# Performance work log

Measured on AMD Instinct MI355X. Metric: run time of the kernel, lower is better.

Reference implementation:

```python
import jax, jax.numpy as jnp
import numpy as np

N_VISITS, N_PROC, N_MED = 64, 32, 16
V_DIAG, V_PROC, V_MED = 2000, 1500, 4000
EMB, EMB_FF = 256, 128


def _normalize(adj):
    # row-normalize(adj + I), matching GCN.normalize
    adj = adj + np.eye(adj.shape[0], dtype=np.float32)
    rs = adj.sum(1)
    rinv = np.where(rs > 0, 1.0 / rs, 0.0).astype(np.float32)
    return (adj * rinv[:, None]).astype(np.float32)


def setup_inputs() -> dict:
    key = jax.random.key(0)
    ks = jax.random.split(key, 24)
    rng = np.random.default_rng(0)
    ehr = (rng.random((V_MED, V_MED)) < 0.01).astype(np.float32)
    ddi = (rng.random((V_MED, V_MED)) < 0.01).astype(np.float32)
    s = 0.02
    return {
        'proc_codes': jax.random.randint(ks[0], (N_VISITS, N_PROC), 0, V_DIAG + V_PROC + 2),
        'med_codes': jax.random.randint(ks[1], (N_VISITS, N_MED), 0, V_MED),
        'emb_table': jax.random.normal(ks[2], (V_DIAG + V_PROC + 2, EMB_FF)) * s,
        'conv_w': jax.random.normal(ks[3], (3,)) * 0.3,
        'conv_b': jnp.zeros((1,)),
        'wq': jax.random.normal(ks[4], (EMB_FF, EMB)) * s,
        'wk': jax.random.normal(ks[5], (EMB_FF, EMB)) * s,
        'wv': jax.random.normal(ks[6], (EMB_FF, EMB)) * s,
        'wr': jax.random.normal(ks[7], (EMB, EMB)) * s,
        'alpha': jax.random.normal(ks[8], (EMB,)),
        'beta': jax.random.normal(ks[9], (EMB,)),
        'ehr_adj_norm': jnp.asarray(_normalize(ehr)),
        'ddi_adj_norm': jnp.asarray(_normalize(ddi)),
        'ddi_adj_raw': jnp.asarray(ddi),
        'ehr_w1': jax.random.normal(ks[10], (V_MED, EMB)) * s,
        'ehr_b1': jnp.zeros((EMB,)),
        'ehr_w2': jax.random.normal(ks[11], (EMB, EMB)) * s,
        'ehr_b2': jnp.zeros((EMB,)),
        'ddi_w1': jax.random.normal(ks[12], (V_MED, EMB)) * s,
        'ddi_b1': jnp.zeros((EMB,)),
        'ddi_w2': jax.random.normal(ks[13], (EMB, EMB)) * s,
        'ddi_b2': jnp.zeros((EMB,)),
        'inter': jax.random.normal(ks[14], (1,)) * 0.1,
        'out_w1': jax.random.normal(ks[15], (3 * EMB, 2 * EMB)) * s,
        'out_b1': jnp.zeros((2 * EMB,)),
        'out_w2': jax.random.normal(ks[16], (2 * EMB, V_MED)) * s,
        'out_b2': jnp.zeros((V_MED,)),
    }


def _fastformer(x, wq, wk, wv, wr, alpha, beta):
    # x: (1, n, EMB_FF); additive linear attention (all-ones mask => no-op)
    q = x @ wq  # (1, n, EMB)
    k = x @ wk
    v = x @ wv
    scale = EMB ** -0.5
    aw = jax.nn.softmax(q * alpha * scale, axis=-1)
    gq = jnp.sum(q * aw, axis=1)              # global query (1, EMB)
    p = gq[:, None, :] * k                    # (1, n, EMB)
    bw = jax.nn.softmax(p * beta * scale, axis=-1)
    gk = jnp.sum(p * bw, axis=1)              # global key (1, EMB)
    return (gk[:, None, :] * v) @ wr + q


def _gcn(adj, w1, b1, w2, b2):
    # input x = I, so first layer support is just w1
    h = jax.nn.relu(adj @ w1 + b1)
    return adj @ (h @ w2) + b2


def reference(proc_codes, med_codes, emb_table, conv_w, conv_b, wq, wk, wv, wr, alpha, beta,
              ehr_adj_norm, ddi_adj_norm, ddi_adj_raw,
              ehr_w1, ehr_b1, ehr_w2, ehr_b2, ddi_w1, ddi_b1, ddi_w2, ddi_b2,
              inter, out_w1, out_b1, out_w2, out_b2):
    n = proc_codes.shape[0]
    # per-admission mean embedding  (n, EMB_FF)
    i2 = emb_table[proc_codes].mean(axis=1)
    # Conv1d(1,1,k=3,same) over the feature dim, then ReLU
    xp = jnp.pad(i2, ((0, 0), (1, 1)))
    i2 = jax.nn.relu(conv_w[0] * xp[:, :-2] + conv_w[1] * xp[:, 1:-1] + conv_w[2] * xp[:, 2:] + conv_b)
    feat = _fastformer(i2[None], wq, wk, wv, wr, alpha, beta)[0]  # (n, EMB)
    query = feat[-1:]
    drug_memory = _gcn(ehr_adj_norm, ehr_w1, ehr_b1, ehr_w2, ehr_b2) \
        - _gcn(ddi_adj_norm, ddi_w1, ddi_b1, ddi_w2, ddi_b2) * inter[0]
    key_w1 = jax.nn.softmax(query @ drug_memory.T, axis=-1)   # (1, V_MED)
    fact1 = key_w1 @ drug_memory                              # (1, EMB)
    # history (len(input) > 1): multi-hot med history values
    history_keys = feat[:-1]
    hv = jnp.zeros((n - 1, V_MED), dtype=feat.dtype)
    hv = hv.at[jnp.arange(n - 1)[:, None], med_codes[:-1]].set(1.0)
    visit_w = jax.nn.softmax(query @ history_keys.T, axis=-1)
    fact2 = (visit_w @ hv) @ drug_memory
    h = jnp.concatenate([query, fact1, fact2], axis=-1)       # (1, 3*EMB)
    result = jax.nn.relu(h @ out_w1 + out_b1) @ out_w2 + out_b2
    sp = jax.nn.sigmoid(result)[0]
    batch_neg = 0.0005 * jnp.einsum('i,ij,j->', sp, ddi_adj_raw, sp)
    return result, batch_neg
```

## Files before the change

kernel.cpp:

```cpp
#include <hip/hip_runtime.h>
#include <hip/hip_bf16.h>

#define NV 64
#define NP 32
#define NM 16
#define VMED 4000
#define EMB 256
#define EMBFF 128
#define CAP 128


__device__ __forceinline__ float block_sum_256(float v, float* red) {
    int t = threadIdx.x;
    red[t] = v; __syncthreads();
    for (int s = 128; s > 0; s >>= 1) { if (t < s) red[t] += red[t + s]; __syncthreads(); }
    float r = red[0]; __syncthreads();
    return r;
}
__device__ __forceinline__ float block_max_256(float v, float* red) {
    int t = threadIdx.x;
    red[t] = v; __syncthreads();
    for (int s = 128; s > 0; s >>= 1) { if (t < s) red[t] = fmaxf(red[t], red[t + s]); __syncthreads(); }
    float r = red[0]; __syncthreads();
    return r;
}

__global__ void k_ff1(const int* __restrict__ proc, const float* __restrict__ emb,
                      const float* __restrict__ cw, const float* __restrict__ cb,
                      const float* __restrict__ wq, const float* __restrict__ wk,
                      const float* __restrict__ wv, const float* __restrict__ alpha,
                      float* __restrict__ q, float* __restrict__ k, float* __restrict__ v,
                      float* __restrict__ qaw) {
    __shared__ float sm[EMBFF + 2];
    __shared__ float x[EMBFF];
    __shared__ float red[256];
    int vi = blockIdx.x, t = threadIdx.x;
    if (t < EMBFF) {
        float s = 0.f;
        for (int c = 0; c < NP; c++) s += emb[proc[vi * NP + c] * EMBFF + t];
        sm[t + 1] = s * (1.0f / NP);
    }
    if (t == 0) { sm[0] = 0.f; sm[EMBFF + 1] = 0.f; }
    __syncthreads();
    if (t < EMBFF) {
        float o = cw[0] * sm[t] + cw[1] * sm[t + 1] + cw[2] * sm[t + 2] + cb[0];
        x[t] = o > 0.f ? o : 0.f;
    }
    __syncthreads();
    float aq = 0, ak = 0, av = 0;
    for (int e = 0; e < EMBFF; e++) {
        float xe = x[e];
        aq += xe * wq[e * EMB + t];
        ak += xe * wk[e * EMB + t];
        av += xe * wv[e * EMB + t];
    }
    q[vi * EMB + t] = aq; k[vi * EMB + t] = ak; v[vi * EMB + t] = av;
    const float scale = 0.0625f;
    float z = aq * alpha[t] * scale;
    float m = block_max_256(z, red);
    float e_ = __expf(z - m);
    float sum = block_sum_256(e_, red);
    qaw[vi * EMB + t] = aq * (e_ / sum);
}

__global__ void k_pbw(const float* __restrict__ qaw, const float* __restrict__ k,
                      const float* __restrict__ beta, float* __restrict__ pbw) {
    __shared__ float red[256];
    int vi = blockIdx.x, f = threadIdx.x;
    float g = 0;
    for (int r = 0; r < NV; r++) g += qaw[r * EMB + f];
    float p = g * k[vi * EMB + f];
    const float scale = 0.0625f;
    float z = p * beta[f] * scale;
    float m = block_max_256(z, red);
    float e_ = __expf(z - m);
    float sum = block_sum_256(e_, red);
    pbw[vi * EMB + f] = p * (e_ / sum);
}

__global__ void k_feat(const float* __restrict__ pbw, const float* __restrict__ v,
                       const float* __restrict__ q, const float* __restrict__ wr,
                       float* __restrict__ feat) {
    __shared__ float s[EMB];
    int vi = blockIdx.x, f = threadIdx.x;
    float g = 0;
    for (int r = 0; r < NV; r++) g += pbw[r * EMB + f];
    s[f] = g * v[vi * EMB + f];
    __syncthreads();
    float acc = 0;
    for (int e = 0; e < EMB; e++) acc += s[e] * wr[e * EMB + f];
    feat[vi * EMB + f] = acc + q[vi * EMB + f];
}

__global__ void k_visitw_wmed(const float* __restrict__ feat, const int* __restrict__ med,
                              float* __restrict__ w_med) {
    __shared__ float qs[EMB];
    __shared__ float vw[64];
    __shared__ float red[256];
    __shared__ float wm[VMED];
    int t = threadIdx.x;
    for (int e = t; e < EMB; e += 256) qs[e] = feat[63 * EMB + e];
    for (int i = t; i < VMED; i += 256) wm[i] = 0.f;
    __syncthreads();
    float sc = -1e30f;
    if (t < 63) {
        float a = 0;
        for (int e = 0; e < EMB; e++) a += qs[e] * feat[t * EMB + e];
        sc = a;
    }
    float m = block_max_256(sc, red);
    float e_ = (t < 63) ? __expf(sc - m) : 0.f;
    float sum = block_sum_256(e_, red);
    if (t < 63) vw[t] = e_ / sum;
    __syncthreads();
    for (int i = t; i < 63 * NM; i += 256) {
        int vv = i / NM, mm = i % NM;
        int code = med[vv * NM + mm];
        bool dup = false;
        for (int m2 = 0; m2 < mm; m2++)
            if (med[vv * NM + m2] == code) dup = true;
        if (!dup) atomicAdd(&wm[code], vw[vv]);
    }
    __syncthreads();
    for (int i = t; i < VMED; i += 256) w_med[i] = wm[i];
}

__global__ void k_qproj(const float* __restrict__ ew2, const float* __restrict__ dw2,
                        const float* __restrict__ b2e, const float* __restrict__ b2d,
                        const float* __restrict__ feat,
                        float* __restrict__ qE, float* __restrict__ qD,
                        float* __restrict__ cc) {
    __shared__ float red[256];
    int b = blockIdx.x, t = threadIdx.x;
    const float* q = feat + 63 * EMB;
    float val;
    if (b < 256)      val = ew2[b * EMB + t] * q[t];
    else if (b < 512) val = dw2[(b - 256) * EMB + t] * q[t];
    else if (b == 512) val = b2e[t] * q[t];
    else               val = b2d[t] * q[t];
    float s = block_sum_256(val, red);
    if (t == 0) {
        if (b < 256) qE[b] = s;
        else if (b < 512) qD[b - 256] = s;
        else if (b == 512) cc[0] = s;
        else cc[1] = s;
    }
}

__global__ void k_scan(const float* __restrict__ eadj, const float* __restrict__ draw,
                       int* __restrict__ ccntE, int* __restrict__ cidxE, float* __restrict__ cvalE,
                       int* __restrict__ ccntD, int* __restrict__ cidxD, float* __restrict__ cvalD) {
    __shared__ int idx[CAP];
    __shared__ float val[CAP];
    __shared__ int cnt;
    int b = blockIdx.x, t = threadIdx.x;
    bool isD = b >= VMED;
    int i = isD ? b - VMED : b;
    const float* adj = isD ? draw : eadj;
    int*   ccnt = isD ? ccntD : ccntE;
    int*   cidx = isD ? cidxD : cidxE;
    float* cval = isD ? cvalD : cvalE;
    if (t == 0) cnt = 0;
    const float4* row4 = (const float4*)(adj + (size_t)i * VMED);
    float4 a0 = row4[t];
    float4 a1 = row4[t + 256];
    float4 a2 = row4[t + 512];
    float4 a3 = (t < VMED / 4 - 768) ? row4[t + 768] : make_float4(0.f, 0.f, 0.f, 0.f);
    asm volatile("" :: "v"(a0.x), "v"(a0.y), "v"(a0.z), "v"(a0.w),
                       "v"(a1.x), "v"(a1.y), "v"(a1.z), "v"(a1.w),
                       "v"(a2.x), "v"(a2.y), "v"(a2.z), "v"(a2.w),
                       "v"(a3.x), "v"(a3.y), "v"(a3.z), "v"(a3.w));
    __syncthreads();
    #define PROC(A, C0) \
        if (A.x != 0.f) { int p = atomicAdd(&cnt, 1); if (p < CAP) { idx[p] = (C0);     val[p] = A.x; } } \
        if (A.y != 0.f) { int p = atomicAdd(&cnt, 1); if (p < CAP) { idx[p] = (C0) + 1; val[p] = A.y; } } \
        if (A.z != 0.f) { int p = atomicAdd(&cnt, 1); if (p < CAP) { idx[p] = (C0) + 2; val[p] = A.z; } } \
        if (A.w != 0.f) { int p = atomicAdd(&cnt, 1); if (p < CAP) { idx[p] = (C0) + 3; val[p] = A.w; } }
    PROC(a0, t * 4)
    PROC(a1, (t + 256) * 4)
    PROC(a2, (t + 512) * 4)
    PROC(a3, (t + 768) * 4)
    #undef PROC
    __syncthreads();
    int n;
    float rinv = 0.f;
    if (isD) {
        int n_raw = cnt < CAP - 1 ? cnt : CAP - 1;
        n = n_raw + 1;
        rinv = 1.0f / (float)n;
        if (t == n_raw) { idx[t] = i; }
    } else {
        n = cnt < CAP ? cnt : CAP;
    }
    __syncthreads();
    int n8 = (n + 7) & ~7;
    if (t == 0) ccnt[i] = n;
    if (t < n)       { cidx[i * CAP + t] = idx[t]; cval[i * CAP + t] = isD ? rinv : val[t]; }
    else if (t < n8) { cidx[i * CAP + t] = 0;      cval[i * CAP + t] = 0.f; }
}

__global__ void k_gat(const int* __restrict__ ccntE, const int* __restrict__ cidxE,
                      const float* __restrict__ cvalE,
                      const int* __restrict__ ccntD, const int* __restrict__ cidxD,
                      const float* __restrict__ cvalD,
                      const float* __restrict__ ew1, const float* __restrict__ eb1,
                      const float* __restrict__ dw1, const float* __restrict__ db1,
                      float* __restrict__ hE, float* __restrict__ hD) {
    int b = blockIdx.x, t = threadIdx.x;
    bool isD = (b & 4) != 0;
    int rank = (b >> 3) * 4 + (b & 3);
    const int*   ccnt = isD ? ccntD : ccntE;
    const int*   cidx = isD ? cidxD : cidxE;
    const float* cval = isD ? cvalD : cvalE;
    const float* w1   = isD ? dw1 : ew1;
    const float* b1   = isD ? db1 : eb1;
    float* h = isD ? hD : hE;
    int r0 = rank * 4;
    for (int r = 0; r < 4; r++) {
        int base = (r0 + r) * CAP;
        int n8 = (ccnt[r0 + r] + 7) & ~7;
        float acc = b1[t];
        for (int e = 0; e < n8; e += 8) {
            int i0 = cidx[base + e];     float v0 = cval[base + e];
            int i1 = cidx[base + e + 1]; float v1 = cval[base + e + 1];
            int i2 = cidx[base + e + 2]; float v2 = cval[base + e + 2];
            int i3 = cidx[base + e + 3]; float v3 = cval[base + e + 3];
            int i4 = cidx[base + e + 4]; float v4 = cval[base + e + 4];
            int i5 = cidx[base + e + 5]; float v5 = cval[base + e + 5];
            int i6 = cidx[base + e + 6]; float v6 = cval[base + e + 6];
            int i7 = cidx[base + e + 7]; float v7 = cval[base + e + 7];
            acc += v0 * w1[(size_t)i0 * EMB + t] + v1 * w1[(size_t)i1 * EMB + t]
                 + v2 * w1[(size_t)i2 * EMB + t] + v3 * w1[(size_t)i3 * EMB + t]
                 + v4 * w1[(size_t)i4 * EMB + t] + v5 * w1[(size_t)i5 * EMB + t]
                 + v6 * w1[(size_t)i6 * EMB + t] + v7 * w1[(size_t)i7 * EMB + t];
        }
        h[(size_t)(r0 + r) * EMB + t] = acc > 0.f ? acc : 0.f;
    }
}

__global__ void k_u(const float* __restrict__ hE, const float* __restrict__ hD,
                    const float* __restrict__ qE, const float* __restrict__ qD,
                    const float* __restrict__ wm,
                    float* __restrict__ uE, float* __restrict__ uD,
                    float* __restrict__ vbuf, float* __restrict__ swm) {
    __shared__ float red[256];
    int b = blockIdx.x, t = threadIdx.x;
    if (b < 2000) {
        int w = t >> 6, lane = t & 63;
        int j = b * 4 + w;
        const float* row; const float* qv; float* uo;
        if (j < VMED) { row = hE + (size_t)j * EMB; qv = qE; uo = uE + j; }
        else { row = hD + (size_t)(j - VMED) * EMB; qv = qD; uo = uD + (j - VMED); }
        float4 hv = *(const float4*)(row + lane * 4);
        float4 qq = *(const float4*)(qv + lane * 4);
        float s = hv.x * qq.x + hv.y * qq.y + hv.z * qq.z + hv.w * qq.w;
        for (int off = 32; off > 0; off >>= 1) s += __shfl_down(s, off, 64);
        if (lane == 0) *uo = s;
    } else if (b < 2063) {
        int idx = (b - 2000) * 256 + t;
        if (idx < 16000) vbuf[idx] = 0.f;
    } else {
        float s = 0;
        for (int i = t; i < VMED; i += 256) s += wm[i];
        s = block_sum_256(s, red);
        if (t == 0) swm[0] = s;
    }
}

__global__ void k_sdm(const int* __restrict__ ccntE, const int* __restrict__ cidxE,
                      const float* __restrict__ cvalE,
                      const int* __restrict__ ccntD, const int* __restrict__ cidxD,
                      const float* __restrict__ cvalD,
                      const float* __restrict__ uE, const float* __restrict__ uD,
                      const float* __restrict__ cc, const float* __restrict__ inter,
                      float* __restrict__ sdm) {
    int t = threadIdx.x;
    int i = blockIdx.x * 4 + (t >> 6), lane = t & 63;
    int nE = ccntE[i];
    float sE = 0.f;
    for (int e = lane; e < nE; e += 64) sE += cvalE[i * CAP + e] * uE[cidxE[i * CAP + e]];
    int nD = ccntD[i];
    float sD = 0.f;
    for (int e = lane; e < nD; e += 64) sD += cvalD[i * CAP + e] * uD[cidxD[i * CAP + e]];
    for (int off = 32; off > 0; off >>= 1) {
        sE += __shfl_down(sE, off, 64);
        sD += __shfl_down(sD, off, 64);
    }
    if (lane == 0) sdm[i] = (sE + cc[0]) - inter[0] * (sD + cc[1]);
}

__global__ void k_softmax4000(const float* __restrict__ s, float* __restrict__ out) {
    __shared__ float red[256];
    int t = threadIdx.x;
    float m = -1e30f;
    for (int i = t; i < VMED; i += 256) m = fmaxf(m, s[i]);
    m = block_max_256(m, red);
    float sum = 0;
    for (int i = t; i < VMED; i += 256) { float e = __expf(s[i] - m); out[i] = e; sum += e; }
    sum = block_sum_256(sum, red);
    float inv = 1.f / sum;
    for (int i = t; i < VMED; i += 256) out[i] *= inv;
}

__global__ void k_scatter(const int* __restrict__ ccntE, const int* __restrict__ cidxE,
                          const float* __restrict__ cvalE,
                          const int* __restrict__ ccntD, const int* __restrict__ cidxD,
                          const float* __restrict__ cvalD,
                          const float* __restrict__ kw, const float* __restrict__ wm,
                          float* __restrict__ vE, float* __restrict__ v2E,
                          float* __restrict__ vD, float* __restrict__ v2D) {
    int t = threadIdx.x;
    int i = blockIdx.x * 4 + (t >> 6), lane = t & 63;
    float kwi = kw[i], wmi = wm[i];
    int nE = ccntE[i];
    for (int e = lane; e < nE; e += 64) {
        int j = cidxE[i * CAP + e];
        float v = cvalE[i * CAP + e];
        atomicAdd(&vE[j], kwi * v);
        atomicAdd(&v2E[j], wmi * v);
    }
    int nD = ccntD[i];
    for (int e = lane; e < nD; e += 64) {
        int j = cidxD[i * CAP + e];
        float v = cvalD[i * CAP + e];
        atomicAdd(&vD[j], kwi * v);
        atomicAdd(&v2D[j], wmi * v);
    }
}

__global__ void k_wsum(const float* __restrict__ hE, const float* __restrict__ hD,
                       const float* __restrict__ vE, const float* __restrict__ v2E,
                       const float* __restrict__ vD, const float* __restrict__ v2D,
                       float* __restrict__ pe1, float* __restrict__ pe2,
                       float* __restrict__ pd1, float* __restrict__ pd2) {
    int f = threadIdx.x, b = blockIdx.x;
    float a1 = 0, a2 = 0, a3 = 0, a4 = 0;
    int j0 = b * 100;
    for (int j = j0; j < j0 + 100; j++) {
        float he = hE[(size_t)j * EMB + f];
        float hd = hD[(size_t)j * EMB + f];
        a1 += vE[j] * he; a2 += v2E[j] * he;
        a3 += vD[j] * hd; a4 += v2D[j] * hd;
    }
    pe1[b * EMB + f] = a1; pe2[b * EMB + f] = a2;
    pd1[b * EMB + f] = a3; pd2[b * EMB + f] = a4;
}

__global__ void k_facts_final(const float* __restrict__ pe1, const float* __restrict__ pe2,
                              const float* __restrict__ pd1, const float* __restrict__ pd2,
                              const float* __restrict__ ew2, const float* __restrict__ dw2,
                              const float* __restrict__ b2e, const float* __restrict__ b2d,
                              const float* __restrict__ inter, const float* __restrict__ swm,
                              float* __restrict__ fact1, float* __restrict__ fact2) {
    __shared__ float gA[EMB];
    __shared__ float gB[EMB];
    int b = blockIdx.x, t = threadIdx.x;
    const float* pa = (b == 0) ? pe1 : pe2;
    const float* pb = (b == 0) ? pd1 : pd2;
    float s1 = 0, s2 = 0;
    for (int p = 0; p < 40; p++) { s1 += pa[p * EMB + t]; s2 += pb[p * EMB + t]; }
    gA[t] = s1; gB[t] = s2;
    __syncthreads();
    float accE = 0, accD = 0;
    for (int e = 0; e < EMB; e++) {
        accE += gA[e] * ew2[e * EMB + t];
        accD += gB[e] * dw2[e * EMB + t];
    }
    float bs = (b == 0) ? 1.f : swm[0];
    float r = accE + bs * b2e[t] - inter[0] * (accD + bs * b2d[t]);
    if (b == 0) fact1[t] = r; else fact2[t] = r;
}

__global__ void k_hidden_part(const float* __restrict__ feat, const float* __restrict__ fact1,
                              const float* __restrict__ fact2, const float* __restrict__ w1,
                              float* __restrict__ hpart) {
    __shared__ float xs[16];
    int b = blockIdx.x, t = threadIdx.x;
    int e0 = b * 16;
    if (t < 16) {
        int e = e0 + t;
        float xv;
        if (e < 256) xv = feat[63 * EMB + e];
        else if (e < 512) xv = fact1[e - 256];
        else              xv = fact2[e - 512];
        xs[t] = xv;
    }
    __syncthreads();
    float a1 = 0, a2 = 0;
    #pragma unroll
    for (int i = 0; i < 16; i++) {
        int e = e0 + i;
        a1 += xs[i] * w1[e * 512 + t];
        a2 += xs[i] * w1[e * 512 + t + 256];
    }
    hpart[b * 512 + t] = a1;
    hpart[b * 512 + t + 256] = a2;
}

__global__ void k_result(const float* __restrict__ hpart, const float* __restrict__ b1,
                         const float* __restrict__ w2, const float* __restrict__ b2,
                         float* __restrict__ out, float* __restrict__ sp) {
    __shared__ float hx[512];
    __shared__ float red[8][32];
    int t = threadIdx.x;
    for (int jj = t; jj < 512; jj += 256) {
        float s = b1[jj];
        for (int p = 0; p < 48; p++) s += hpart[p * 512 + jj];
        hx[jj] = s > 0.f ? s : 0.f;
    }
    __syncthreads();
    int lane = t & 31, seg = t >> 5;
    int j = blockIdx.x * 32 + lane;
    float acc = 0;
    int e0 = seg * 64;
    #pragma unroll 8
    for (int e = e0; e < e0 + 64; e++) acc += hx[e] * w2[(size_t)e * VMED + j];
    red[seg][lane] = acc;
    __syncthreads();
    if (seg == 0) {
        float s = b2[j];
        for (int p = 0; p < 8; p++) s += red[p][lane];
        out[j] = s;
        sp[j] = 1.f / (1.f + __expf(-s));
    }
}

__global__ void k_bneg(const int* __restrict__ ccntD, const int* __restrict__ cidxD,
                       const float* __restrict__ sp, float* __restrict__ bpart) {
    int wv = threadIdx.x >> 6, lane = threadIdx.x & 63;
    int i = blockIdx.x * 4 + wv;
    int n = ccntD[i] - 1;
    float s = 0.f;
    for (int e = lane; e < n; e += 64) s += sp[cidxD[i * CAP + e]];
    for (int off = 32; off > 0; off >>= 1) s += __shfl_down(s, off, 64);
    if (lane == 0) bpart[i] = sp[i] * s;
}

__global__ void FastRx_wo_Diag_19473381720179_kernel(const float* __restrict__ bpart,
                                                     float* __restrict__ out) {
    __shared__ float red[256];
    int t = threadIdx.x;
    float s = 0;
    for (int i = t; i < VMED; i += 256) s += bpart[i];
    s = block_sum_256(s, red);
    if (t == 0) out[VMED] = 0.0005f * s;
}

extern "C" __attribute__((visibility("default")))
void kernel_launch(void* const* d_in, const int* in_sizes, int n_in,
                   void* d_out, int out_size, void* d_ws, size_t ws_size,
                   hipStream_t stream) {
    const int*   proc_codes = (const int*)d_in[0];
    const int*   med_codes  = (const int*)d_in[1];
    const float* emb_table  = (const float*)d_in[2];
    const float* conv_w     = (const float*)d_in[3];
    const float* conv_b     = (const float*)d_in[4];
    const float* wq         = (const float*)d_in[5];
    const float* wk         = (const float*)d_in[6];
    const float* wv         = (const float*)d_in[7];
    const float* wr         = (const float*)d_in[8];
    const float* alpha      = (const float*)d_in[9];
    const float* beta       = (const float*)d_in[10];
    const float* ehr_adj    = (const float*)d_in[11];
    const float* ddi_adj    = (const float*)d_in[12];
    const float* ddi_raw    = (const float*)d_in[13];
    const float* ehr_w1     = (const float*)d_in[14];
    const float* ehr_b1     = (const float*)d_in[15];
    const float* ehr_w2     = (const float*)d_in[16];
    const float* ehr_b2     = (const float*)d_in[17];
    const float* ddi_w1     = (const float*)d_in[18];
    const float* ddi_b1     = (const float*)d_in[19];
    const float* ddi_w2     = (const float*)d_in[20];
    const float* ddi_b2     = (const float*)d_in[21];
    const float* inter      = (const float*)d_in[22];
    const float* out_w1     = (const float*)d_in[23];
    const float* out_b1     = (const float*)d_in[24];
    const float* out_w2     = (const float*)d_in[25];
    const float* out_b2     = (const float*)d_in[26];
    float* out = (float*)d_out;

    float* w = (float*)d_ws;
    float* q      = w;
    float* k      = w + 16384;
    float* v      = w + 32768;
    float* tmpA   = w + 49152;
    float* tmpB   = w + 65536;
    float* feat   = w + 81920;
    float* wmed   = w + 98304;
    float* sdm    = w + 102400;
    float* sp     = w + 106496;
    float* bufA   = w + 110592;
    float* bufC   = bufA + 1024000;
    float* bufB   = bufC + 1024000;
    int*   ccntE  = (int*)(bufB + 1024000);
    int*   cidxE  = ccntE + 4096;
    float* cvalE  = (float*)(cidxE + 512000);
    int*   ccntD  = (int*)(cvalE + 512000);
    int*   cidxD  = ccntD + 4096;
    float* cvalD  = (float*)(cidxD + 512000);
    float* qE   = bufB;
    float* qD   = bufB + 256;
    float* cc   = bufB + 512;
    float* swm  = bufB + 514;
    float* uE   = bufB + 1024;
    float* uD   = bufB + 5120;
    float* vbuf = bufB + 10240;
    float* vE   = vbuf;
    float* v2E  = vbuf + 4000;
    float* vD   = vbuf + 8000;
    float* v2D  = vbuf + 12000;
    float* pe1  = bufB + 26624;
    float* pe2  = bufB + 36864;
    float* pd1  = bufB + 47104;
    float* pd2  = bufB + 57344;
    float* fact1  = bufA;
    float* fact2  = bufA + 256;
    float* hpart  = bufA + 20480;
    float* bpart  = bufA + 45056;

    k_ff1<<<NV, EMB, 0, stream>>>(proc_codes, emb_table, conv_w, conv_b,
                                  wq, wk, wv, alpha, q, k, v, tmpA);
    k_pbw<<<NV, EMB, 0, stream>>>(tmpA, k, beta, tmpB);
    k_feat<<<NV, EMB, 0, stream>>>(tmpB, v, q, wr, feat);
    k_visitw_wmed<<<1, 256, 0, stream>>>(feat, med_codes, wmed);
    k_qproj<<<514, 256, 0, stream>>>(ehr_w2, ddi_w2, ehr_b2, ddi_b2, feat, qE, qD, cc);

    k_scan<<<2 * VMED, 256, 0, stream>>>(ehr_adj, ddi_raw,
                                         ccntE, cidxE, cvalE, ccntD, cidxD, cvalD);
    k_gat<<<2000, 256, 0, stream>>>(ccntE, cidxE, cvalE, ccntD, cidxD, cvalD,
                                    ehr_w1, ehr_b1, ddi_w1, ddi_b1,
                                    bufA, bufC);
    k_u<<<2064, 256, 0, stream>>>(bufA, bufC, qE, qD, wmed, uE, uD, vbuf, swm);
    k_sdm<<<1000, 256, 0, stream>>>(ccntE, cidxE, cvalE, ccntD, cidxD, cvalD,
                                    uE, uD, cc, inter, sdm);
    k_softmax4000<<<1, 256, 0, stream>>>(sdm, sdm);
    k_scatter<<<1000, 256, 0, stream>>>(ccntE, cidxE, cvalE, ccntD, cidxD, cvalD,
                                        sdm, wmed, vE, v2E, vD, v2D);
    k_wsum<<<40, 256, 0, stream>>>(bufA, bufC, vE, v2E, vD, v2D, pe1, pe2, pd1, pd2);
    k_facts_final<<<2, 256, 0, stream>>>(pe1, pe2, pd1, pd2, ehr_w2, ddi_w2,
                                         ehr_b2, ddi_b2, inter, swm, fact1, fact2);
    k_hidden_part<<<48, 256, 0, stream>>>(feat, fact1, fact2, out_w1, hpart);
    k_result<<<125, 256, 0, stream>>>(hpart, out_b1, out_w2, out_b2, out, sp);
    k_bneg<<<VMED / 4, 256, 0, stream>>>(ccntD, cidxD, sp, bpart);
    FastRx_wo_Diag_19473381720179_kernel<<<1, 256, 0, stream>>>(bpart, out);
}
```

Before: 402.4 us.

## Fuse small kernels to cut launch count and split wsum across more blocks

Merges visit-weight/med-weight and query projection into one k_mid launch, which also zeroes vbuf and computes the wm sum. The u dot products move into k_gat's epilogue through a block reduction, so k_u goes away. k_hidden_part is folded into k_result, where all 125 blocks recompute the 768x512 hidden layer redundantly. k_wsum is split into 160 blocks, one accumulator each. The aim is to remove launch overhead and raise parallelism, at the cost of redundant hidden-layer work and extra syncs in k_gat.

```diff
diff --git a/kernel.cpp b/kernel.cpp
--- a/kernel.cpp
+++ b/kernel.cpp
@@ -92,58 +92,65 @@
     feat[vi * EMB + f] = acc + q[vi * EMB + f];
 }
 
-__global__ void k_visitw_wmed(const float* __restrict__ feat, const int* __restrict__ med,
-                              float* __restrict__ w_med) {
+__global__ void k_mid(const float* __restrict__ feat, const int* __restrict__ med,
+                      const float* __restrict__ ew2, const float* __restrict__ dw2,
+                      const float* __restrict__ b2e, const float* __restrict__ b2d,
+                      float* __restrict__ w_med, float* __restrict__ swm,
+                      float* __restrict__ qE, float* __restrict__ qD,
+                      float* __restrict__ cc, float* __restrict__ vbuf) {
     __shared__ float qs[EMB];
     __shared__ float vw[64];
     __shared__ float red[256];
     __shared__ float wm[VMED];
-    int t = threadIdx.x;
-    for (int e = t; e < EMB; e += 256) qs[e] = feat[63 * EMB + e];
-    for (int i = t; i < VMED; i += 256) wm[i] = 0.f;
-    __syncthreads();
-    float sc = -1e30f;
-    if (t < 63) {
-        float a = 0;
-        for (int e = 0; e < EMB; e++) a += qs[e] * feat[t * EMB + e];
-        sc = a;
-    }
-    float m = block_max_256(sc, red);
-    float e_ = (t < 63) ? __expf(sc - m) : 0.f;
-    float sum = block_sum_256(e_, red);
-    if (t < 63) vw[t] = e_ / sum;
-    __syncthreads();
-    for (int i = t; i < 63 * NM; i += 256) {
-        int vv = i / NM, mm = i % NM;
-        int code = med[vv * NM + mm];
-        bool dup = false;
-        for (int m2 = 0; m2 < mm; m2++)
-            if (med[vv * NM + m2] == code) dup = true;
-        if (!dup) atomicAdd(&wm[code], vw[vv]);
-    }
-    __syncthreads();
-    for (int i = t; i < VMED; i += 256) w_med[i] = wm[i];
-}
-
-__global__ void k_qproj(const float* __restrict__ ew2, const float* __restrict__ dw2,
-                        const float* __restrict__ b2e, const float* __restrict__ b2d,
-                        const float* __restrict__ feat,
-                        float* __restrict__ qE, float* __restrict__ qD,
-                        float* __restrict__ cc) {
-    __shared__ float red[256];
     int b = blockIdx.x, t = threadIdx.x;
-    const float* q = feat + 63 * EMB;
-    float val;
-    if (b < 256)      val = ew2[b * EMB + t] * q[t];
-    else if (b < 512) val = dw2[(b - 256) * EMB + t] * q[t];
-    else if (b == 512) val = b2e[t] * q[t];
-    else               val = b2d[t] * q[t];
-    float s = block_sum_256(val, red);
-    if (t == 0) {
-        if (b < 256) qE[b] = s;
-        else if (b < 512) qD[b - 256] = s;
-        else if (b == 512) cc[0] = s;
-        else cc[1] = s;
+    if (b == 0) {
+        for (int e = t; e < EMB; e += 256) qs[e] = feat[63 * EMB + e];
+        for (int i = t; i < VMED; i += 256) wm[i] = 0.f;
+        __syncthreads();
+        float sc = -1e30f;
+        if (t < 63) {
+            float a = 0;
+            for (int e = 0; e < EMB; e++) a += qs[e] * feat[t * EMB + e];
+            sc = a;
+        }
+        float m = block_max_256(sc, red);
+        float e_ = (t < 63) ? __expf(sc - m) : 0.f;
+        float sum = block_sum_256(e_, red);
+        if (t < 63) vw[t] = e_ / sum;
+        __syncthreads();
+        for (int i = t; i < 63 * NM; i += 256) {
+            int vv = i / NM, mm = i % NM;
+            int code = med[vv * NM + mm];
+            bool dup = false;
+            for (int m2 = 0; m2 < mm; m2++)
+                if (med[vv * NM + m2] == code) dup = true;
+            if (!dup) atomicAdd(&wm[code], vw[vv]);
+        }
+        __syncthreads();
+        for (int i = t; i < VMED; i += 256) w_med[i] = wm[i];
+        __syncthreads();
+        float s = 0;
+        for (int i = t; i < VMED; i += 256) s += wm[i];
+        s = block_sum_256(s, red);
+        if (t == 0) swm[0] = s;
+    } else if (b <= 514) {
+        int bb = b - 1;
+        const float* q = feat + 63 * EMB;
+        float val;
+        if (bb < 256)       val = ew2[bb * EMB + t] * q[t];
+        else if (bb < 512)  val = dw2[(bb - 256) * EMB + t] * q[t];
+        else if (bb == 512) val = b2e[t] * q[t];
+        else                val = b2d[t] * q[t];
+        float s = block_sum_256(val, red);
+        if (t == 0) {
+            if (bb < 256) qE[bb] = s;
+            else if (bb < 512) qD[bb - 256] = s;
+            else if (bb == 512) cc[0] = s;
+            else cc[1] = s;
+        }
+    } else {
+        int idx = (b - 515) * 256 + t;
+        if (idx < 16000) vbuf[idx] = 0.f;
     }
 }
 
@@ -205,7 +212,10 @@
                       const float* __restrict__ cvalD,
                       const float* __restrict__ ew1, const float* __restrict__ eb1,
                       const float* __restrict__ dw1, const float* __restrict__ db1,
-                      float* __restrict__ hE, float* __restrict__ hD) {
+                      const float* __restrict__ qE, const float* __restrict__ qD,
+                      float* __restrict__ hE, float* __restrict__ hD,
+                      float* __restrict__ uE, float* __restrict__ uD) {
+    __shared__ float red[256];
     int b = blockIdx.x, t = threadIdx.x;
     bool isD = (b & 4) != 0;
     int rank = (b >> 3) * 4 + (b & 3);
@@ -215,6 +225,8 @@
     const float* w1   = isD ? dw1 : ew1;
     const float* b1   = isD ? db1 : eb1;
     float* h = isD ? hD : hE;
+    float* u = isD ? uD : uE;
+    float qt = (isD ? qD : qE)[t];
     int r0 = rank * 4;
     for (int r = 0; r < 4; r++) {
         int base = (r0 + r) * CAP;
@@ -234,36 +246,10 @@
                  + v4 * w1[(size_t)i4 * EMB + t] + v5 * w1[(size_t)i5 * EMB + t]
                  + v6 * w1[(size_t)i6 * EMB + t] + v7 * w1[(size_t)i7 * EMB + t];
         }
-        h[(size_t)(r0 + r) * EMB + t] = acc > 0.f ? acc : 0.f;
-    }
-}
-
-__global__ void k_u(const float* __restrict__ hE, const float* __restrict__ hD,
-                    const float* __restrict__ qE, const float* __restrict__ qD,
-                    const float* __restrict__ wm,
-                    float* __restrict__ uE, float* __restrict__ uD,
-                    float* __restrict__ vbuf, float* __restrict__ swm) {
-    __shared__ float red[256];
-    int b = blockIdx.x, t = threadIdx.x;
-    if (b < 2000) {
-        int w = t >> 6, lane = t & 63;
-        int j = b * 4 + w;
-        const float* row; const float* qv; float* uo;
-        if (j < VMED) { row = hE + (size_t)j * EMB; qv = qE; uo = uE + j; }
-        else { row = hD + (size_t)(j - VMED) * EMB; qv = qD; uo = uD + (j - VMED); }
-        float4 hv = *(const float4*)(row + lane * 4);
-        float4 qq = *(const float4*)(qv + lane * 4);
-        float s = hv.x * qq.x + hv.y * qq.y + hv.z * qq.z + hv.w * qq.w;
-        for (int off = 32; off > 0; off >>= 1) s += __shfl_down(s, off, 64);
-        if (lane == 0) *uo = s;
-    } else if (b < 2063) {
-        int idx = (b - 2000) * 256 + t;
-        if (idx < 16000) vbuf[idx] = 0.f;
-    } else {
-        float s = 0;
-        for (int i = t; i < VMED; i += 256) s += wm[i];
-        s = block_sum_256(s, red);
-        if (t == 0) swm[0] = s;
+        float hr = acc > 0.f ? acc : 0.f;
+        h[(size_t)(r0 + r) * EMB + t] = hr;
+        float s = block_sum_256(hr * qt, red);
+        if (t == 0) u[r0 + r] = s;
     }
 }
 
@@ -334,16 +320,18 @@
                        float* __restrict__ pe1, float* __restrict__ pe2,
                        float* __restrict__ pd1, float* __restrict__ pd2) {
     int f = threadIdx.x, b = blockIdx.x;
-    float a1 = 0, a2 = 0, a3 = 0, a4 = 0;
-    int j0 = b * 100;
-    for (int j = j0; j < j0 + 100; j++) {
-        float he = hE[(size_t)j * EMB + f];
-        float hd = hD[(size_t)j * EMB + f];
-        a1 += vE[j] * he; a2 += v2E[j] * he;
-        a3 += vD[j] * hd; a4 += v2D[j] * hd;
-    }
-    pe1[b * EMB + f] = a1; pe2[b * EMB + f] = a2;
-    pd1[b * EMB + f] = a3; pd2[b * EMB + f] = a4;
+    int a = b / 40, chunk = b % 40;
+    const float* h; const float* v; float* p;
+    if (a == 0)      { h = hE; v = vE;  p = pe1; }
+    else if (a == 1) { h = hE; v = v2E; p = pe2; }
+    else if (a == 2) { h = hD; v = vD;  p = pd1; }
+    else             { h = hD; v = v2D; p = pd2; }
+    float acc = 0;
+    int j0 = chunk * 100;
+    #pragma unroll 4
+    for (int j = j0; j < j0 + 100; j++)
+        acc += v[j] * h[(size_t)j * EMB + f];
+    p[chunk * EMB + f] = acc;
 }
 
 __global__ void k_facts_final(const float* __restrict__ pe1, const float* __restrict__ pe2,
@@ -371,41 +359,29 @@
     if (b == 0) fact1[t] = r; else fact2[t] = r;
 }
 
-__global__ void k_hidden_part(const float* __restrict__ feat, const float* __restrict__ fact1,
-                              const float* __restrict__ fact2, const float* __restrict__ w1,
-                              float* __restrict__ hpart) {
-    __shared__ float xs[16];
-    int b = blockIdx.x, t = threadIdx.x;
-    int e0 = b * 16;
-    if (t < 16) {
-        int e = e0 + t;
-        float xv;
-        if (e < 256) xv = feat[63 * EMB + e];
-        else if (e < 512) xv = fact1[e - 256];
-        else              xv = fact2[e - 512];
-        xs[t] = xv;
-    }
-    __syncthreads();
-    float a1 = 0, a2 = 0;
-    #pragma unroll
-    for (int i = 0; i < 16; i++) {
-        int e = e0 + i;
-        a1 += xs[i] * w1[e * 512 + t];
-        a2 += xs[i] * w1[e * 512 + t + 256];
-    }
-    hpart[b * 512 + t] = a1;
-    hpart[b * 512 + t + 256] = a2;
-}
-
-__global__ void k_result(const float* __restrict__ hpart, const float* __restrict__ b1,
+__global__ void k_result(const float* __restrict__ feat, const float* __restrict__ fact1,
+                         const float* __restrict__ fact2, const float* __restrict__ w1,
+                         const float* __restrict__ b1,
                          const float* __restrict__ w2, const float* __restrict__ b2,
                          float* __restrict__ out, float* __restrict__ sp) {
+    __shared__ float xs[768];
     __shared__ float hx[512];
     __shared__ float red[8][32];
     int t = threadIdx.x;
+    xs[t] = feat[63 * EMB + t];
+    xs[256 + t] = fact1[t];
+    xs[512 + t] = fact2[t];
+    __syncthreads();
     for (int jj = t; jj < 512; jj += 256) {
         float s = b1[jj];
-        for (int p = 0; p < 48; p++) s += hpart[p * 512 + jj];
+        for (int p = 0; p < 48; p++) {
+            int e0 = p * 16;
+            float partial = 0;
+            #pragma unroll
+            for (int i = 0; i < 16; i++)
+                partial += xs[e0 + i] * w1[(e0 + i) * 512 + jj];
+            s += partial;
+        }
         hx[jj] = s > 0.f ? s : 0.f;
     }
     __syncthreads();
@@ -515,32 +491,30 @@
     float* pd2  = bufB + 57344;
     float* fact1  = bufA;
     float* fact2  = bufA + 256;
-    float* hpart  = bufA + 20480;
     float* bpart  = bufA + 45056;
 
     k_ff1<<<NV, EMB, 0, stream>>>(proc_codes, emb_table, conv_w, conv_b,
                                   wq, wk, wv, alpha, q, k, v, tmpA);
     k_pbw<<<NV, EMB, 0, stream>>>(tmpA, k, beta, tmpB);
     k_feat<<<NV, EMB, 0, stream>>>(tmpB, v, q, wr, feat);
-    k_visitw_wmed<<<1, 256, 0, stream>>>(feat, med_codes, wmed);
-    k_qproj<<<514, 256, 0, stream>>>(ehr_w2, ddi_w2, ehr_b2, ddi_b2, feat, qE, qD, cc);
+    k_mid<<<578, 256, 0, stream>>>(feat, med_codes, ehr_w2, ddi_w2, ehr_b2, ddi_b2,
+                                   wmed, swm, qE, qD, cc, vbuf);
 
     k_scan<<<2 * VMED, 256, 0, stream>>>(ehr_adj, ddi_raw,
                                          ccntE, cidxE, cvalE, ccntD, cidxD, cvalD);
     k_gat<<<2000, 256, 0, stream>>>(ccntE, cidxE, cvalE, ccntD, cidxD, cvalD,
                                     ehr_w1, ehr_b1, ddi_w1, ddi_b1,
-                                    bufA, bufC);
-    k_u<<<2064, 256, 0, stream>>>(bufA, bufC, qE, qD, wmed, uE, uD, vbuf, swm);
+                                    qE, qD, bufA, bufC, uE, uD);
     k_sdm<<<1000, 256, 0, stream>>>(ccntE, cidxE, cvalE, ccntD, cidxD, cvalD,
                                     uE, uD, cc, inter, sdm);
     k_softmax4000<<<1, 256, 0, stream>>>(sdm, sdm);
     k_scatter<<<1000, 256, 0, stream>>>(ccntE, cidxE, cvalE, ccntD, cidxD, cvalD,
                                         sdm, wmed, vE, v2E, vD, v2D);
-    k_wsum<<<40, 256, 0, stream>>>(bufA, bufC, vE, v2E, vD, v2D, pe1, pe2, pd1, pd2);
+    k_wsum<<<160, 256, 0, stream>>>(bufA, bufC, vE, v2E, vD, v2D, pe1, pe2, pd1, pd2);
     k_facts_final<<<2, 256, 0, stream>>>(pe1, pe2, pd1, pd2, ehr_w2, ddi_w2,
                                          ehr_b2, ddi_b2, inter, swm, fact1, fact2);
-    k_hidden_part<<<48, 256, 0, stream>>>(feat, fact1, fact2, out_w1, hpart);
-    k_result<<<125, 256, 0, stream>>>(hpart, out_b1, out_w2, out_b2, out, sp);
+    k_result<<<125, 256, 0, stream>>>(feat, fact1, fact2, out_w1, out_b1,
+                                      out_w2, out_b2, out, sp);
     k_bneg<<<VMED / 4, 256, 0, stream>>>(ccntD, cidxD, sp, bpart);
     FastRx_wo_Diag_19473381720179_kernel<<<1, 256, 0, stream>>>(bpart, out);
 }
```

After: 442.4 us. 9.9% more time.
